# Kernel optimization log

Hardware: AMD Instinct MI355X
Metric: run time of the kernel (lower is better)

## Reference

```python
import jax, jax.numpy as jnp
import numpy as np

# Closed-form 2-qubit circuit: |00> -> RY(a) on q0, RY(b) on q1 -> CNOT(0,1) -> RY(theta) on q0,
# then measure <Z0>,<Z1>, output (Z+1)/2. torchquantum wire0 = most significant bit.

PIXELS = 3072
N_PAIRS = 460
N_CLASSES = 10
BATCH = 1024


def setup_inputs() -> dict:
    key = jax.random.key(0)
    k1, k2, k3 = jax.random.split(key, 3)
    x = jax.random.normal(k1, (BATCH, 3, 32, 32), dtype=jnp.float32)
    theta = jax.random.normal(k2, (N_CLASSES,), dtype=jnp.float32)  # per-class RY angle
    pair_idx = jax.random.randint(k3, (BATCH, N_PAIRS, 2), 0, PIXELS)
    return {"x": x, "theta": theta, "pair_idx": pair_idx}


def reference(x, theta, pair_idx):
    B = x.shape[0]
    flat = x.reshape(B, -1)  # [B, 3072]
    # gather paired pixel values: [B, P, 2]
    vals = jnp.take_along_axis(flat, pair_idx.reshape(B, -1), axis=1).reshape(B, N_PAIRS, 2)
    a = vals[..., 0]  # angle for qubit 0
    b = vals[..., 1]  # angle for qubit 1
    ca, sa = jnp.cos(a / 2), jnp.sin(a / 2)
    cb, sb = jnp.cos(b / 2), jnp.sin(b / 2)
    # state after RY(a)xRY(b) then CNOT(ctrl=0, tgt=1): swap |10><->|11>
    psi00 = ca * cb
    psi01 = ca * sb
    psi10 = sa * sb  # was psi11
    psi11 = sa * cb  # was psi10
    # RY(theta) on qubit 0, per class: broadcast [B,P,1] x [C]
    ct = jnp.cos(theta / 2)[None, None, :]
    st = jnp.sin(theta / 2)[None, None, :]
    p00 = ct * psi00[..., None] - st * psi10[..., None]
    p10 = st * psi00[..., None] + ct * psi10[..., None]
    p01 = ct * psi01[..., None] - st * psi11[..., None]
    p11 = st * psi01[..., None] + ct * psi11[..., None]
    q00, q01, q10, q11 = p00 * p00, p01 * p01, p10 * p10, p11 * p11
    z0 = q00 + q01 - q10 - q11  # <Z> on wire 0
    z1 = q00 - q01 + q10 - q11  # <Z> on wire 1
    qout = (jnp.stack([z0, z1], axis=2) + 1.0) / 2.0  # [B, P, 2, C]
    return qout.reshape(B, N_PAIRS * 2, N_CLASSES)
```

## Files before the change

### kernel.cpp

```cpp
#include <hip/hip_runtime.h>

#define NPAIRS 460
#define NCLASS 10
#define PIX    3072
#define BATCH  1024
#define TPB    512
#define OPAD   21

__global__ __launch_bounds__(TPB) void
qmem_kernel(const float* __restrict__ x,
            const float* __restrict__ theta,
            const int2*  __restrict__ pidx,
            float* __restrict__ out)
{
    __shared__ float s_x[PIX];
    __shared__ float s_out[NPAIRS * OPAD];
    __shared__ float s_ct[NCLASS], s_st[NCLASS];

    const int b = blockIdx.x;
    const int t = threadIdx.x;

    const float2* xrow = (const float2*)(x + (size_t)b * PIX);
#pragma unroll
    for (int i = 0; i < 3; ++i) {
        int j = t + i * TPB;
        float2 v = xrow[j];
        s_x[2 * j]     = v.x;
        s_x[2 * j + 1] = v.y;
    }
    if (t < NCLASS) {
        float s, c;
        __sincosf(theta[t], &s, &c);
        s_ct[t] = c;
        s_st[t] = s;
    }
    __syncthreads();

    if (t < NPAIRS) {
        int2 pi = pidx[(size_t)b * NPAIRS + t];
        float av = s_x[pi.x];
        float bv = s_x[pi.y];
        float sa, ca, sb, cb;
        __sincosf(av, &sa, &ca);
        __sincosf(bv, &sb, &cb);
        float sasb = sa * sb;
        float o1   = fmaf(0.5f, ca * cb, 0.5f);
        float* po  = s_out + t * OPAD;
#pragma unroll
        for (int c = 0; c < NCLASS; ++c)
            po[c] = fmaf(0.5f, s_ct[c] * ca - s_st[c] * sasb, 0.5f);
#pragma unroll
        for (int c = NCLASS; c < 2 * NCLASS; ++c)
            po[c] = o1;
    }
    __syncthreads();

    float4* og = (float4*)(out + (size_t)b * (NPAIRS * 2 * NCLASS));
    for (int j = t; j < NPAIRS * 5; j += TPB) {
        int p = j / 5;
        int k = (j - p * 5) * 4;
        const float* ps = s_out + p * OPAD + k;
        og[j] = make_float4(ps[0], ps[1], ps[2], ps[3]);
    }
}

extern "C" void kernel_launch(void* const* d_in, const int* in_sizes, int n_in,
                              void* d_out, int out_size, void* d_ws, size_t ws_size,
                              hipStream_t stream) {
    const float* x     = (const float*)d_in[0];
    const float* theta = (const float*)d_in[1];
    const int2*  pidx  = (const int2*)d_in[2];
    float* out = (float*)d_out;

    qmem_kernel<<<BATCH, TPB, 0, stream>>>(x, theta, pidx, out);
}
```

Before: 15.16 us.

## Compute outputs directly per float4 slot, dropping shared-memory output staging

Each thread now computes the four output values for its float4 slot straight from the shared pixel row and shared pair indices, then writes them to global memory, removing the padded shared output buffer and the second barrier. The work is spread over all 512 threads instead of 460 threads followed by a copy pass. In exchange, sincos is recomputed up to five times per pair, and the class index becomes dynamic, which can make the theta coefficient lookups less efficient. Freeing shared memory may also raise occupancy.

```diff
diff --git a/kernel.cpp b/kernel.cpp
--- a/kernel.cpp
+++ b/kernel.cpp
@@ -5,16 +5,16 @@
 #define PIX    3072
 #define BATCH  1024
 #define TPB    512
-#define OPAD   21
+#define NF4    (NPAIRS * 5)
 
 __global__ __launch_bounds__(TPB) void
 qmem_kernel(const float* __restrict__ x,
             const float* __restrict__ theta,
             const int2*  __restrict__ pidx,
-            float* __restrict__ out)
+            float4* __restrict__ out)
 {
     __shared__ float s_x[PIX];
-    __shared__ float s_out[NPAIRS * OPAD];
+    __shared__ int2  s_pi[NPAIRS];
     __shared__ float s_ct[NCLASS], s_st[NCLASS];
 
     const int b = blockIdx.x;
@@ -28,6 +28,8 @@
         s_x[2 * j]     = v.x;
         s_x[2 * j + 1] = v.y;
     }
+    const int2* prow = pidx + (size_t)b * NPAIRS;
+    if (t < NPAIRS) s_pi[t] = prow[t];
     if (t < NCLASS) {
         float s, c;
         __sincosf(theta[t], &s, &c);
@@ -36,31 +38,29 @@
     }
     __syncthreads();
 
-    if (t < NPAIRS) {
-        int2 pi = pidx[(size_t)b * NPAIRS + t];
-        float av = s_x[pi.x];
-        float bv = s_x[pi.y];
+    float4* og = out + (size_t)b * NF4;
+    for (int j = t; j < NF4; j += TPB) {
+        int p = j / 5;
+        int k = (j - p * 5) * 4;
+        int2 pi = s_pi[p];
         float sa, ca, sb, cb;
-        __sincosf(av, &sa, &ca);
-        __sincosf(bv, &sb, &cb);
+        __sincosf(s_x[pi.x], &sa, &ca);
+        __sincosf(s_x[pi.y], &sb, &cb);
         float sasb = sa * sb;
         float o1   = fmaf(0.5f, ca * cb, 0.5f);
-        float* po  = s_out + t * OPAD;
+
+        float4 v;
+        float* vp = (float*)&v;
 #pragma unroll
-        for (int c = 0; c < NCLASS; ++c)
-            po[c] = fmaf(0.5f, s_ct[c] * ca - s_st[c] * sasb, 0.5f);
-#pragma unroll
-        for (int c = NCLASS; c < 2 * NCLASS; ++c)
-            po[c] = o1;
-    }
-    __syncthreads();
-
-    float4* og = (float4*)(out + (size_t)b * (NPAIRS * 2 * NCLASS));
-    for (int j = t; j < NPAIRS * 5; j += TPB) {
-        int p = j / 5;
-        int k = (j - p * 5) * 4;
-        const float* ps = s_out + p * OPAD + k;
-        og[j] = make_float4(ps[0], ps[1], ps[2], ps[3]);
+        for (int e = 0; e < 4; ++e) {
+            int c = k + e;
+            if (c < NCLASS) {
+                vp[e] = fmaf(0.5f, s_ct[c] * ca - s_st[c] * sasb, 0.5f);
+            } else {
+                vp[e] = o1;
+            }
+        }
+        og[j] = v;
     }
 }
 
@@ -70,7 +70,7 @@
     const float* x     = (const float*)d_in[0];
     const float* theta = (const float*)d_in[1];
     const int2*  pidx  = (const int2*)d_in[2];
-    float* out = (float*)d_out;
+    float4* out = (float4*)d_out;
 
     qmem_kernel<<<BATCH, TPB, 0, stream>>>(x, theta, pidx, out);
 }
```

Measured after the change: 14.98 us. No clear change (-1.2%).
